# Performance work log

Measured on AMD Instinct MI355X. Metric: run time of the kernel, lower is better.

The kernel has to match this reference:

```python
import jax, jax.numpy as jnp
import numpy as np

ALPHA_1 = 0.5
ALPHA_2 = 0.9
TAU = 0.1
BIG_NUM = 1.0e9


def setup_inputs() -> dict:
    key = jax.random.key(0)
    k1, k2 = jax.random.split(key)
    B, N_SUP, N_QRY, D = 4, 512, 4096, 128
    features = jax.random.normal(k1, (B, N_SUP + N_QRY, D), dtype=jnp.float32)
    support_labels = jax.random.randint(k2, (B, N_SUP), 0, 64, dtype=jnp.int64)
    return {"features": features, "support_labels": support_labels}


def _sq_dists(x, y):
    # squared Euclidean pairwise distances: [B, N, M]
    xn = jnp.sum(x * x, axis=-1)  # [B, N]
    yn = jnp.sum(y * y, axis=-1)  # [B, M]
    xy = jnp.einsum('bnd,bmd->bnm', x, y)
    return xn[:, :, None] + yn[:, None, :] - 2.0 * xy


def reference(features, support_labels):
    n_support = support_labels.shape[1]
    support = features[:, :n_support]   # [B, S, D]
    query = features[:, n_support:]     # [B, Q, D]

    # --- re_represent_queries ---
    logits = -TAU * _sq_dists(query, query)           # [B, Q, Q]
    Q = query.shape[1]
    rng = jnp.arange(Q)
    logits = logits.at[:, rng, rng].set(-BIG_NUM)     # mask self-similarity
    attn_q = jax.nn.softmax(logits, axis=2)
    # Faithful to source: (attn[:,:,:,None] * q[:,:,None,:]).sum(2)
    # i.e. row index of q matches row index of attn; softmax axis j is contracted
    # against a broadcast copy of the same row.
    re_rep_q = jnp.einsum('bij,bid->bid', attn_q, query)
    new_query = (1.0 - ALPHA_1) * query + ALPHA_1 * re_rep_q

    # --- re_represent_supports ---
    logits_s = -TAU * _sq_dists(support, new_query)   # [B, S, Q]
    attn_s = jax.nn.softmax(logits_s, axis=2)
    re_rep_s = jnp.einsum('bsq,bqd->bsd', attn_s, new_query)
    new_support = (1.0 - ALPHA_2) * support + ALPHA_2 * re_rep_s

    return jnp.concatenate((new_support, new_query), axis=1)
```

## Files before the change

### kernel.cpp

```cpp
#include <hip/hip_runtime.h>

#define BATCH 4
#define NS 512
#define NQ 4096
#define D 128
#define NTOT (NS + NQ)

#define NCHUNK 16
#define QCHUNK (NQ / NCHUNK)
#define QT 64
#define ST 64
#define PITN 136
#define PITT 72

typedef __attribute__((ext_vector_type(8))) short bf16x8;
typedef __attribute__((ext_vector_type(4))) float f32x4;

#define L2E 1.4426950408889634f
#define SCL 0.28853900817779268f

__device__ __forceinline__ unsigned short f2bf(float f) {
    unsigned int x = __float_as_uint(f);
    return (unsigned short)((x + 0x7fffu + ((x >> 16) & 1u)) >> 16);
}

__global__ __launch_bounds__(256) void attend_kernel(const float* __restrict__ feat,
                                                     float* __restrict__ out,
                                                     float* __restrict__ accP,
                                                     float* __restrict__ lsumP) {
    __shared__ unsigned short qn_[QT * PITN];
    __shared__ unsigned short qt_[D * PITT];
    __shared__ unsigned short p_[ST * PITT];
    __shared__ float qns[QCHUNK];

    int chunk = blockIdx.x, stile = blockIdx.y, b = blockIdx.z;
    int s0 = stile * ST;
    int q0 = chunk * QCHUNK;
    int t = threadIdx.x;
    int w = t >> 6, ln = t & 15, quad = (t >> 4) & 3;

    const float* srow = feat + ((size_t)b * NTOT + s0 + 16 * w + ln) * D;
    bf16x8 asup[4];
    #pragma unroll
    for (int kk = 0; kk < 4; ++kk) {
        float4 lo = *(const float4*)(srow + 32 * kk + 8 * quad);
        float4 hi = *(const float4*)(srow + 32 * kk + 8 * quad + 4);
        union { bf16x8 v; unsigned short u[8]; } pk;
        pk.u[0] = f2bf(lo.x); pk.u[1] = f2bf(lo.y); pk.u[2] = f2bf(lo.z); pk.u[3] = f2bf(lo.w);
        pk.u[4] = f2bf(hi.x); pk.u[5] = f2bf(hi.y); pk.u[6] = f2bf(hi.z); pk.u[7] = f2bf(hi.w);
        asup[kk] = pk.v;
    }

    f32x4 cpv[8];
    #pragma unroll
    for (int ds = 0; ds < 8; ++ds) cpv[ds] = (f32x4){0.f, 0.f, 0.f, 0.f};
    float lpart[4] = {0.f, 0.f, 0.f, 0.f};

    int qrow = t >> 2;
    int dgrp = (t & 3) * 4;
    const float* qchunk_base = feat + ((size_t)b * NTOT + NS + q0) * D;
    float* outq = out + ((size_t)b * NTOT + NS + q0) * D;
    int copy_qt = (stile >> 1) << 6;
    int copy_ok = (qrow >> 5) == (stile & 1);

    for (int qt = 0; qt < QCHUNK; qt += QT) {
        __syncthreads();
        const float* qbase = qchunk_base + (size_t)(qt + qrow) * D;
        float nrm = 0.f;
        int docopy = (qt == copy_qt) & copy_ok;
        #pragma unroll
        for (int i = 0; i < 8; ++i) {
            int d = dgrp + 16 * i;
            float4 v = *(const float4*)(qbase + d);
            if (docopy) *(float4*)(outq + (size_t)(qt + qrow) * D + d) = v;
            nrm += v.x * v.x + v.y * v.y + v.z * v.z + v.w * v.w;
            unsigned short b0 = f2bf(v.x), b1 = f2bf(v.y), b2 = f2bf(v.z), b3 = f2bf(v.w);
            *(unsigned int*)&qn_[qrow * PITN + d]     = (unsigned)b0 | ((unsigned)b1 << 16);
            *(unsigned int*)&qn_[qrow * PITN + d + 2] = (unsigned)b2 | ((unsigned)b3 << 16);
            qt_[(d + 0) * PITT + qrow] = b0;
            qt_[(d + 1) * PITT + qrow] = b1;
            qt_[(d + 2) * PITT + qrow] = b2;
            qt_[(d + 3) * PITT + qrow] = b3;
        }
        nrm += __shfl_xor(nrm, 1, 64);
        nrm += __shfl_xor(nrm, 2, 64);
        if ((t & 3) == 0) qns[qt + qrow] = 0.1f * L2E * nrm;
        __syncthreads();

        f32x4 cqk[4];
        #pragma unroll
        for (int f = 0; f < 4; ++f) cqk[f] = (f32x4){0.f, 0.f, 0.f, 0.f};
        #pragma unroll
        for (int kk = 0; kk < 4; ++kk) {
            #pragma unroll
            for (int f = 0; f < 4; ++f) {
                bf16x8 bq = *(const bf16x8*)&qn_[(16 * f + ln) * PITN + 32 * kk + 8 * quad];
                cqk[f] = __builtin_amdgcn_mfma_f32_16x16x32_bf16(asup[kk], bq, cqk[f], 0, 0, 0);
            }
        }

        #pragma unroll
        for (int f = 0; f < 4; ++f) {
            float qs = qns[qt + 16 * f + ln];
            #pragma unroll
            for (int r = 0; r < 4; ++r) {
                float e = exp2f(SCL * cqk[f][r] - qs);
                lpart[r] += e;
                p_[(16 * w + 4 * quad + r) * PITT + 16 * f + ln] = f2bf(e);
            }
        }
        __syncthreads();

        #pragma unroll
        for (int kk = 0; kk < 2; ++kk) {
            bf16x8 ap = *(const bf16x8*)&p_[(16 * w + ln) * PITT + 32 * kk + 8 * quad];
            #pragma unroll
            for (int ds = 0; ds < 8; ++ds) {
                bf16x8 bv = *(const bf16x8*)&qt_[(16 * ds + ln) * PITT + 32 * kk + 8 * quad];
                cpv[ds] = __builtin_amdgcn_mfma_f32_16x16x32_bf16(ap, bv, cpv[ds], 0, 0, 0);
            }
        }
    }

    int base = (chunk * BATCH + b) * NS + s0;
    #pragma unroll
    for (int r = 0; r < 4; ++r) {
        float v = lpart[r];
        v += __shfl_xor(v, 1, 64);
        v += __shfl_xor(v, 2, 64);
        v += __shfl_xor(v, 4, 64);
        v += __shfl_xor(v, 8, 64);
        if (ln == 0) lsumP[base + 16 * w + 4 * quad + r] = v;
    }
    #pragma unroll
    for (int ds = 0; ds < 8; ++ds)
        #pragma unroll
        for (int r = 0; r < 4; ++r)
            accP[(size_t)(base + 16 * w + 4 * quad + r) * D + 16 * ds + ln] = cpv[ds][r];
}

__global__ __launch_bounds__(256) void epi_kernel(const float* __restrict__ feat,
                                                  const float* __restrict__ accP,
                                                  const float* __restrict__ lsumP,
                                                  float* __restrict__ out) {
    int wave = threadIdx.x >> 6;
    int lane = threadIdx.x & 63;
    int row = blockIdx.x * 4 + wave;
    int b = row >> 9;
    int s = row & (NS - 1);

    float l = 0.f, ax = 0.f, ay = 0.f;
    #pragma unroll 4
    for (int c = 0; c < NCHUNK; ++c) {
        int base = (c * BATCH + b) * NS + s;
        l += lsumP[base];
        float2 a = *(const float2*)(accP + (size_t)base * D + lane * 2);
        ax += a.x; ay += a.y;
    }
    float inv = 0.9f / l;
    size_t fo = ((size_t)b * NTOT + s) * D + lane * 2;
    float2 sup = *(const float2*)(feat + fo);
    float2 o;
    o.x = 0.1f * sup.x + ax * inv;
    o.y = 0.1f * sup.y + ay * inv;
    *(float2*)(out + fo) = o;
}

extern "C" void kernel_launch(void* const* d_in, const int* in_sizes, int n_in,
                              void* d_out, int out_size, void* d_ws, size_t ws_size,
                              hipStream_t stream) {
    const float* feat = (const float*)d_in[0];
    float* out = (float*)d_out;
    float* ws = (float*)d_ws;
    float* accP  = ws;
    float* lsumP = accP + (size_t)NCHUNK * BATCH * NS * D;
    (void)in_sizes; (void)n_in; (void)out_size; (void)ws_size;

    attend_kernel<<<dim3(NCHUNK, NS / ST, BATCH), 256, 0, stream>>>(feat, out, accP, lsumP);
    epi_kernel<<<BATCH * NS / 4, 256, 0, stream>>>(feat, accP, lsumP, out);
}
```

Before: 85.64 us.

## Double support tile per block so each wave reuses query fragments twice

Each block now handles 128 support rows instead of 64. Every wave carries two 16-row M-tiles, so each query bf16 fragment loaded from LDS feeds two MFMAs. Query tile staging (global loads, bf16 conversion, transpose into LDS) is amortized over twice as many support rows, and the grid shrinks from 512 to 256 blocks. The cost is roughly double the accumulator and A-fragment registers, which may lower occupancy, and fewer blocks to spread across CUs. The query copy-through is reassigned so each of the 4 support tiles copies one full 64-row query tile.

```diff
diff --git a/kernel.cpp b/kernel.cpp
--- a/kernel.cpp
+++ b/kernel.cpp
@@ -9,7 +9,7 @@
 #define NCHUNK 16
 #define QCHUNK (NQ / NCHUNK)
 #define QT 64
-#define ST 64
+#define ST 128
 #define PITN 136
 #define PITT 72
 
@@ -39,35 +39,39 @@
     int t = threadIdx.x;
     int w = t >> 6, ln = t & 15, quad = (t >> 4) & 3;
 
-    const float* srow = feat + ((size_t)b * NTOT + s0 + 16 * w + ln) * D;
-    bf16x8 asup[4];
-    #pragma unroll
-    for (int kk = 0; kk < 4; ++kk) {
-        float4 lo = *(const float4*)(srow + 32 * kk + 8 * quad);
-        float4 hi = *(const float4*)(srow + 32 * kk + 8 * quad + 4);
-        union { bf16x8 v; unsigned short u[8]; } pk;
-        pk.u[0] = f2bf(lo.x); pk.u[1] = f2bf(lo.y); pk.u[2] = f2bf(lo.z); pk.u[3] = f2bf(lo.w);
-        pk.u[4] = f2bf(hi.x); pk.u[5] = f2bf(hi.y); pk.u[6] = f2bf(hi.z); pk.u[7] = f2bf(hi.w);
-        asup[kk] = pk.v;
+    bf16x8 asup[2][4];
+    #pragma unroll
+    for (int mt = 0; mt < 2; ++mt) {
+        const float* srow = feat + ((size_t)b * NTOT + s0 + 64 * mt + 16 * w + ln) * D;
+        #pragma unroll
+        for (int kk = 0; kk < 4; ++kk) {
+            float4 lo = *(const float4*)(srow + 32 * kk + 8 * quad);
+            float4 hi = *(const float4*)(srow + 32 * kk + 8 * quad + 4);
+            union { bf16x8 v; unsigned short u[8]; } pk;
+            pk.u[0] = f2bf(lo.x); pk.u[1] = f2bf(lo.y); pk.u[2] = f2bf(lo.z); pk.u[3] = f2bf(lo.w);
+            pk.u[4] = f2bf(hi.x); pk.u[5] = f2bf(hi.y); pk.u[6] = f2bf(hi.z); pk.u[7] = f2bf(hi.w);
+            asup[mt][kk] = pk.v;
+        }
     }
 
-    f32x4 cpv[8];
-    #pragma unroll
-    for (int ds = 0; ds < 8; ++ds) cpv[ds] = (f32x4){0.f, 0.f, 0.f, 0.f};
-    float lpart[4] = {0.f, 0.f, 0.f, 0.f};
+    f32x4 cpv[2][8];
+    #pragma unroll
+    for (int mt = 0; mt < 2; ++mt)
+        #pragma unroll
+        for (int ds = 0; ds < 8; ++ds) cpv[mt][ds] = (f32x4){0.f, 0.f, 0.f, 0.f};
+    float lpart[2][4] = {{0.f,0.f,0.f,0.f},{0.f,0.f,0.f,0.f}};
 
     int qrow = t >> 2;
     int dgrp = (t & 3) * 4;
     const float* qchunk_base = feat + ((size_t)b * NTOT + NS + q0) * D;
     float* outq = out + ((size_t)b * NTOT + NS + q0) * D;
-    int copy_qt = (stile >> 1) << 6;
-    int copy_ok = (qrow >> 5) == (stile & 1);
+    int copy_qt = stile * QT;
 
     for (int qt = 0; qt < QCHUNK; qt += QT) {
         __syncthreads();
         const float* qbase = qchunk_base + (size_t)(qt + qrow) * D;
         float nrm = 0.f;
-        int docopy = (qt == copy_qt) & copy_ok;
+        int docopy = (qt == copy_qt);
         #pragma unroll
         for (int i = 0; i < 8; ++i) {
             int d = dgrp + 16 * i;
@@ -87,56 +91,74 @@
         if ((t & 3) == 0) qns[qt + qrow] = 0.1f * L2E * nrm;
         __syncthreads();
 
-        f32x4 cqk[4];
-        #pragma unroll
-        for (int f = 0; f < 4; ++f) cqk[f] = (f32x4){0.f, 0.f, 0.f, 0.f};
+        f32x4 cqk[2][4];
+        #pragma unroll
+        for (int mt = 0; mt < 2; ++mt)
+            #pragma unroll
+            for (int f = 0; f < 4; ++f) cqk[mt][f] = (f32x4){0.f, 0.f, 0.f, 0.f};
         #pragma unroll
         for (int kk = 0; kk < 4; ++kk) {
             #pragma unroll
             for (int f = 0; f < 4; ++f) {
                 bf16x8 bq = *(const bf16x8*)&qn_[(16 * f + ln) * PITN + 32 * kk + 8 * quad];
-                cqk[f] = __builtin_amdgcn_mfma_f32_16x16x32_bf16(asup[kk], bq, cqk[f], 0, 0, 0);
+                #pragma unroll
+                for (int mt = 0; mt < 2; ++mt)
+                    cqk[mt][f] = __builtin_amdgcn_mfma_f32_16x16x32_bf16(asup[mt][kk], bq,
+                                                                         cqk[mt][f], 0, 0, 0);
             }
         }
 
         #pragma unroll
-        for (int f = 0; f < 4; ++f) {
-            float qs = qns[qt + 16 * f + ln];
-            #pragma unroll
-            for (int r = 0; r < 4; ++r) {
-                float e = exp2f(SCL * cqk[f][r] - qs);
-                lpart[r] += e;
-                p_[(16 * w + 4 * quad + r) * PITT + 16 * f + ln] = f2bf(e);
+        for (int mt = 0; mt < 2; ++mt)
+            #pragma unroll
+            for (int f = 0; f < 4; ++f) {
+                float qs = qns[qt + 16 * f + ln];
+                #pragma unroll
+                for (int r = 0; r < 4; ++r) {
+                    float e = exp2f(SCL * cqk[mt][f][r] - qs);
+                    lpart[mt][r] += e;
+                    p_[(64 * mt + 16 * w + 4 * quad + r) * PITT + 16 * f + ln] = f2bf(e);
+                }
             }
-        }
         __syncthreads();
 
         #pragma unroll
         for (int kk = 0; kk < 2; ++kk) {
-            bf16x8 ap = *(const bf16x8*)&p_[(16 * w + ln) * PITT + 32 * kk + 8 * quad];
+            bf16x8 ap[2];
+            #pragma unroll
+            for (int mt = 0; mt < 2; ++mt)
+                ap[mt] = *(const bf16x8*)&p_[(64 * mt + 16 * w + ln) * PITT + 32 * kk + 8 * quad];
             #pragma unroll
             for (int ds = 0; ds < 8; ++ds) {
                 bf16x8 bv = *(const bf16x8*)&qt_[(16 * ds + ln) * PITT + 32 * kk + 8 * quad];
-                cpv[ds] = __builtin_amdgcn_mfma_f32_16x16x32_bf16(ap, bv, cpv[ds], 0, 0, 0);
+                #pragma unroll
+                for (int mt = 0; mt < 2; ++mt)
+                    cpv[mt][ds] = __builtin_amdgcn_mfma_f32_16x16x32_bf16(ap[mt], bv,
+                                                                          cpv[mt][ds], 0, 0, 0);
             }
         }
     }
 
     int base = (chunk * BATCH + b) * NS + s0;
     #pragma unroll
-    for (int r = 0; r < 4; ++r) {
-        float v = lpart[r];
-        v += __shfl_xor(v, 1, 64);
-        v += __shfl_xor(v, 2, 64);
-        v += __shfl_xor(v, 4, 64);
-        v += __shfl_xor(v, 8, 64);
-        if (ln == 0) lsumP[base + 16 * w + 4 * quad + r] = v;
-    }
-    #pragma unroll
-    for (int ds = 0; ds < 8; ++ds)
-        #pragma unroll
-        for (int r = 0; r < 4; ++r)
-            accP[(size_t)(base + 16 * w + 4 * quad + r) * D + 16 * ds + ln] = cpv[ds][r];
+    for (int mt = 0; mt < 2; ++mt)
+        #pragma unroll
+        for (int r = 0; r < 4; ++r) {
+            float v = lpart[mt][r];
+            v += __shfl_xor(v, 1, 64);
+            v += __shfl_xor(v, 2, 64);
+            v += __shfl_xor(v, 4, 64);
+            v += __shfl_xor(v, 8, 64);
+            if (ln == 0) lsumP[base + 64 * mt + 16 * w + 4 * quad + r] = v;
+        }
+    #pragma unroll
+    for (int mt = 0; mt < 2; ++mt)
+        #pragma unroll
+        for (int ds = 0; ds < 8; ++ds)
+            #pragma unroll
+            for (int r = 0; r < 4; ++r)
+                accP[(size_t)(base + 64 * mt + 16 * w + 4 * quad + r) * D + 16 * ds + ln] =
+                    cpv[mt][ds][r];
 }
 
 __global__ __launch_bounds__(256) void epi_kernel(const float* __restrict__ feat,
```

After: 88.56 us. 1.03x slower.
